# Kernel optimization log

Hardware: AMD Instinct MI355X
Metric: run time of the kernel (lower is better)

Reference implementation:

```python
import jax, jax.numpy as jnp
import numpy as np
from jax import lax

B, N, D, H, LAT, N_ENV = 8, 1024, 256, 8, 32, 64
HD = D // H


def _forward(x, conv_w, conv_b, phy_w, phy_b, to_out_w, to_out_b, env_keys,
             env_proj_w, env_proj_b, lambda_, q_w, q_b, k_w, k_b, v_w, v_b,
             out_proj_w, out_proj_b, gate_w, gate_b):
    b, n, d = x.shape
    h = H
    hd = d // h
    scale = hd ** -0.5
    hdim = int(np.sqrt(n))
    wdim = n // hdim

    # ---- physics branch: conv3x3 -> global avg pool -> linear -> 2h scalars ----
    K2d = x.reshape(b, hdim, wdim, d).transpose(0, 3, 1, 2)  # (b, d, H, W)
    conv = lax.conv_general_dilated(K2d, conv_w, (1, 1), ((1, 1), (1, 1)),
                                    dimension_numbers=('NCHW', 'OIHW', 'NCHW'))
    conv = conv + conv_b[None, :, None, None]
    pooled = conv.mean(axis=(2, 3))                 # (b, LAT)
    phy = pooled @ phy_w.T + phy_b                  # (b, 2h)
    atten = phy[:, :h][:, :, None, None]            # (b, h, 1, 1)
    scat = phy[:, h:][:, :, None, None]

    # ---- main physics-modulated attention (q=k=v=x, unprojected) ----
    q = x.reshape(b, n, h, hd).transpose(0, 2, 1, 3)  # (b, h, n, hd)
    k = q * (1.0 / (atten + 1e-6))
    dots = jnp.einsum('bhnd,bhmd->bhnm', q, k) * scale
    dots = dots * scat
    attn = jax.nn.softmax(dots, axis=-1)
    out = jnp.einsum('bhnm,bhmd->bhnd', attn, q)      # v == q here
    out = out.transpose(0, 2, 1, 3).reshape(b, n, d)
    out = out @ to_out_w.T + to_out_b

    # ---- env-memory branch (faithful to source: dim0 treated as tgt_len,
    #      dim1 as batch, so attention runs across the batch axis) ----
    n_env = env_keys.shape[0]
    q_e = (x @ q_w.T + q_b).reshape(b, n * h, hd).transpose(1, 0, 2)  # (n*h, b, hd)
    k_e = (x @ k_w.T + k_b).reshape(b, n * h, hd).transpose(1, 0, 2)
    v_e = (x @ v_w.T + v_b).reshape(b, n * h, hd).transpose(1, 0, 2)
    env_k = env_keys @ env_proj_w.T + env_proj_b                       # (n_env, d)
    env_k_bh = jnp.broadcast_to(env_k[:, None, :], (n_env, n, d))
    env_k_bh = env_k_bh.reshape(n_env, n * h, hd).transpose(1, 0, 2)   # (n*h, n_env, hd)

    attn_score = jnp.einsum('zbd,zcd->zbc', q_e, k_e)                  # (n*h, b, b)
    env_score = jnp.einsum('zbd,zed->zbe', q_e, env_k_bh)              # (n*h, b, n_env)
    combined = jnp.concatenate([attn_score, lambda_ * env_score], axis=-1)
    combined = jax.nn.softmax(combined / (hd ** 0.5), axis=-1)
    aw = combined[..., :b]
    ew = combined[..., b:]

    # env values: note (h, n) flattening order as in source permute/reshape
    env_v = jnp.broadcast_to(env_k.reshape(n_env, h, hd)[:, None, :, :],
                             (n_env, n, h, hd))
    env_v = env_v.transpose(2, 1, 0, 3).reshape(n * h, n_env, hd)

    out_e = jnp.einsum('zbc,zcd->zbd', aw, v_e) + jnp.einsum('zbe,zed->zbd', ew, env_v)
    out_e = out_e.transpose(1, 0, 2).reshape(b, n, d)
    out_e = out_e @ out_proj_w.T + out_proj_b

    # ---- gated fusion ----
    g = jax.nn.sigmoid(jnp.concatenate([out, out_e], axis=-1) @ gate_w.T + gate_b)
    return g * out + (1.0 - g) * out_e


def setup_inputs() -> dict:
    key = jax.random.key(0)
    ks = jax.random.split(key, 16)
    rn = lambda k, s: (jax.random.normal(k, s, dtype=jnp.float32) * 0.02)
    return {
        'x': jax.random.normal(ks[0], (B, N, D), dtype=jnp.float32),
        'conv_w': rn(ks[1], (LAT, D, 3, 3)),
        'conv_b': jnp.zeros((LAT,), jnp.float32),
        'phy_w': rn(ks[2], (2 * H, LAT)),
        'phy_b': jnp.ones((2 * H,), jnp.float32),  # keep attenuation ~1 for stability
        'to_out_w': rn(ks[3], (D, D)),
        'to_out_b': jnp.zeros((D,), jnp.float32),
        'env_keys': jax.random.normal(ks[4], (N_ENV, D), dtype=jnp.float32),
        'env_proj_w': rn(ks[5], (D, D)),
        'env_proj_b': jnp.zeros((D,), jnp.float32),
        'lambda_': jnp.asarray(0.5, jnp.float32),
        'q_w': rn(ks[6], (D, D)), 'q_b': jnp.zeros((D,), jnp.float32),
        'k_w': rn(ks[7], (D, D)), 'k_b': jnp.zeros((D,), jnp.float32),
        'v_w': rn(ks[8], (D, D)), 'v_b': jnp.zeros((D,), jnp.float32),
        'out_proj_w': rn(ks[9], (D, D)),
        'out_proj_b': jnp.zeros((D,), jnp.float32),
        'gate_w': rn(ks[10], (D, 2 * D)),
        'gate_b': jnp.zeros((D,), jnp.float32),
    }


def reference(x, conv_w, conv_b, phy_w, phy_b, to_out_w, to_out_b, env_keys,
              env_proj_w, env_proj_b, lambda_, q_w, q_b, k_w, k_b, v_w, v_b,
              out_proj_w, out_proj_b, gate_w, gate_b):
    return _forward(x, conv_w, conv_b, phy_w, phy_b, to_out_w, to_out_b,
                    env_keys, env_proj_w, env_proj_b, lambda_, q_w, q_b,
                    k_w, k_b, v_w, v_b, out_proj_w, out_proj_b, gate_w, gate_b)
```

## Files before the change

### kernel.cpp

```cpp
#include <hip/hip_runtime.h>
#include <hip/hip_bf16.h>
#include <cstdint>
#include <cstddef>

#define NB 8
#define NN 1024
#define ND 256
#define NH 8
#define HD 32

typedef __attribute__((ext_vector_type(8))) short bf16x8;
typedef __attribute__((ext_vector_type(4))) float f32x4;

static __device__ __forceinline__ float dot4(float4 a, float4 b) {
    return a.x * b.x + a.y * b.y + a.z * b.z + a.w * b.w;
}

static __device__ __forceinline__ uint32_t pack2bf(float x, float y) {
    __hip_bfloat16 bx = __float2bfloat16(x), by = __float2bfloat16(y);
    return (uint32_t)(*reinterpret_cast<uint16_t*>(&bx)) |
           ((uint32_t)(*reinterpret_cast<uint16_t*>(&by)) << 16);
}

static __device__ __forceinline__ ushort bf1(float x) {
    __hip_bfloat16 b = __float2bfloat16(x);
    return *reinterpret_cast<ushort*>(&b);
}

__global__ __launch_bounds__(256) void conv_sums_k(const float* __restrict__ x,
                                                   float* __restrict__ S) {
    const int b = blockIdx.y;
    const int q = blockIdx.x;
    const int c = threadIdx.x;
    const float* xb = x + (size_t)b * (NN * ND) + c;
    float T = 0.f, R0 = 0.f, R31 = 0.f, C0 = 0.f, C31 = 0.f;
    float c00 = 0.f, c0N = 0.f, cN0 = 0.f, cNN = 0.f;
    const int n0 = q * 64;
    for (int nn = 0; nn < 64; ++nn) {
        const int n = n0 + nn;
        const float v = xb[(size_t)n * ND];
        T += v;
        if (n < 32)   R0 += v;
        if (n >= 992) R31 += v;
        const int j = n & 31;
        if (j == 0)  C0 += v;
        if (j == 31) C31 += v;
        if (n == 0)    c00 = v;
        if (n == 31)   c0N = v;
        if (n == 992)  cN0 = v;
        if (n == 1023) cNN = v;
    }
    float* Sp = S + (size_t)b * 2304 + c * 9;
    atomicAdd(&Sp[0], T - R31 - C31 + cNN);
    atomicAdd(&Sp[1], T - R31);
    atomicAdd(&Sp[2], T - R31 - C0 + cN0);
    atomicAdd(&Sp[3], T - C31);
    atomicAdd(&Sp[4], T);
    atomicAdd(&Sp[5], T - C0);
    atomicAdd(&Sp[6], T - R0 - C31 + c0N);
    atomicAdd(&Sp[7], T - R0);
    atomicAdd(&Sp[8], T - R0 - C0 + c00);
}

__global__ __launch_bounds__(64) void pooled_k(const float* __restrict__ S,
                                               const float* __restrict__ conv_w,
                                               const float* __restrict__ conv_b,
                                               float* __restrict__ pooled) {
    const int bx = blockIdx.x;
    const int b = bx >> 5, o = bx & 31;
    const int t = threadIdx.x;
    const float4* w4 = (const float4*)(conv_w + (size_t)o * 2304);
    const float4* s4 = (const float4*)(S + (size_t)b * 2304);
    float acc = 0.f;
#pragma unroll
    for (int f = 0; f < 9; ++f) acc += dot4(w4[f * 64 + t], s4[f * 64 + t]);
    acc += __shfl_xor(acc, 1);  acc += __shfl_xor(acc, 2);
    acc += __shfl_xor(acc, 4);  acc += __shfl_xor(acc, 8);
    acc += __shfl_xor(acc, 16); acc += __shfl_xor(acc, 32);
    if (t == 0) pooled[b * 32 + o] = conv_b[o] + acc * (1.f / 1024.f);
}

__global__ __launch_bounds__(64) void phy_coef_k(const float* __restrict__ pooled,
                                                 const float* __restrict__ phy_w,
                                                 const float* __restrict__ phy_b,
                                                 float* __restrict__ coef) {
    __shared__ float ps[8][32];
    const int t = threadIdx.x;
#pragma unroll
    for (int r = 0; r < 4; ++r) {
        const int idx = r * 64 + t;
        ps[idx >> 5][idx & 31] = pooled[idx];
    }
    __syncthreads();
    const int b = t & 7, hh = t >> 3;
    float atten = phy_b[hh], scat = phy_b[8 + hh];
#pragma unroll
    for (int l = 0; l < 32; ++l) {
        atten += ps[b][l] * phy_w[hh * 32 + l];
        scat  += ps[b][l] * phy_w[(8 + hh) * 32 + l];
    }
    coef[b * 8 + hh] = 0.17677669529663687f * scat / (atten + 1e-6f);
}

__global__ __launch_bounds__(256) void phys_attn_mfma_k(const float* __restrict__ x,
                                                        const float* __restrict__ coef,
                                                        float* __restrict__ attn_out) {
    const int bh = blockIdx.y;
    const int b = bh >> 3, h = bh & 7;
    const int wv = threadIdx.x >> 6, lane = threadIdx.x & 63;
    const int g = lane >> 4, c16 = lane & 15;
    const float cf = coef[bh];
    const float* xb = x + (size_t)b * (NN * ND) + h * HD;

    __shared__ ushort Kl[2][32][40];
    __shared__ ushort VT[2][32][40];

    bf16x8 qf[2];
    const int q0 = blockIdx.x * 128 + wv * 32;
#pragma unroll
    for (int fq = 0; fq < 2; ++fq) {
        const float* qr = xb + (size_t)(q0 + fq * 16 + c16) * ND + g * 8;
        const float4 v0 = *(const float4*)&qr[0];
        const float4 v1 = *(const float4*)&qr[4];
        union { bf16x8 v; uint32_t u[4]; } qq;
        qq.u[0] = pack2bf(v0.x * cf, v0.y * cf);
        qq.u[1] = pack2bf(v0.z * cf, v0.w * cf);
        qq.u[2] = pack2bf(v1.x * cf, v1.y * cf);
        qq.u[3] = pack2bf(v1.z * cf, v1.w * cf);
        qf[fq] = qq.v;
    }

    const int skv = threadIdx.x >> 3, sdq = (threadIdx.x & 7) * 4;
    {
        const float4 v = *(const float4*)&xb[(size_t)skv * ND + sdq];
        const ushort e0 = bf1(v.x), e1 = bf1(v.y), e2 = bf1(v.z), e3 = bf1(v.w);
        uint2 kw; kw.x = (uint32_t)e0 | ((uint32_t)e1 << 16);
        kw.y = (uint32_t)e2 | ((uint32_t)e3 << 16);
        *(uint2*)&Kl[0][skv][sdq] = kw;
        VT[0][sdq + 0][skv] = e0; VT[0][sdq + 1][skv] = e1;
        VT[0][sdq + 2][skv] = e2; VT[0][sdq + 3][skv] = e3;
    }
    __syncthreads();

    f32x4 oacc[2][2];
#pragma unroll
    for (int i = 0; i < 2; ++i)
#pragma unroll
        for (int j = 0; j < 2; ++j) oacc[i][j] = (f32x4){0.f, 0.f, 0.f, 0.f};
    float m[2] = {-3.0e38f, -3.0e38f};
    float lsum[2] = {0.f, 0.f};

    const int srcA = c16 + (((2 * g) & 3) << 4);
    const int srcB = c16 + (((2 * g + 1) & 3) << 4);
    const int srcQ = (lane & 48) | (g * 4);

    for (int c = 0; c < 16 * 2; ++c) {
        const int cur = c & 1;
        float4 nv;
        const bool hasNext = (c + 1 < 32);
        if (hasNext)
            nv = *(const float4*)&xb[(size_t)((c + 1) * 32 + skv) * ND + sdq];

        const bf16x8 af0 = *(const bf16x8*)&Kl[cur][c16][g * 8];
        const bf16x8 af1 = *(const bf16x8*)&Kl[cur][16 + c16][g * 8];
        f32x4 sacc[2][2];
        const f32x4 z4 = (f32x4){0.f, 0.f, 0.f, 0.f};
        sacc[0][0] = __builtin_amdgcn_mfma_f32_16x16x32_bf16(af0, qf[0], z4, 0, 0, 0);
        sacc[0][1] = __builtin_amdgcn_mfma_f32_16x16x32_bf16(af0, qf[1], z4, 0, 0, 0);
        sacc[1][0] = __builtin_amdgcn_mfma_f32_16x16x32_bf16(af1, qf[0], z4, 0, 0, 0);
        sacc[1][1] = __builtin_amdgcn_mfma_f32_16x16x32_bf16(af1, qf[1], z4, 0, 0, 0);

        bf16x8 pa[2];
        float corrS[2];
#pragma unroll
        for (int fq = 0; fq < 2; ++fq) {
            float vmax = sacc[0][fq][0];
#pragma unroll
            for (int j = 1; j < 4; ++j) vmax = fmaxf(vmax, sacc[0][fq][j]);
#pragma unroll
            for (int j = 0; j < 4; ++j) vmax = fmaxf(vmax, sacc[1][fq][j]);
            vmax = fmaxf(vmax, __shfl_xor(vmax, 16));
            vmax = fmaxf(vmax, __shfl_xor(vmax, 32));
            const float mn = fmaxf(m[fq], vmax);
            corrS[fq] = __expf(m[fq] - mn);
            m[fq] = mn;
            float p[2][4];
            float rs = 0.f;
#pragma unroll
            for (int fkv = 0; fkv < 2; ++fkv)
#pragma unroll
                for (int j = 0; j < 4; ++j) {
                    p[fkv][j] = __expf(sacc[fkv][fq][j] - mn);
                    rs += p[fkv][j];
                }
            rs += __shfl_xor(rs, 16);
            rs += __shfl_xor(rs, 32);
            lsum[fq] = lsum[fq] * corrS[fq] + rs;

            uint32_t pk00 = pack2bf(p[0][0], p[0][1]);
            uint32_t pk01 = pack2bf(p[0][2], p[0][3]);
            uint32_t pk10 = pack2bf(p[1][0], p[1][1]);
            uint32_t pk11 = pack2bf(p[1][2], p[1][3]);
            const int t00 = __shfl((int)pk00, srcA), t10 = __shfl((int)pk10, srcA);
            const int t01 = __shfl((int)pk01, srcA), t11 = __shfl((int)pk11, srcA);
            const int t02 = __shfl((int)pk00, srcB), t12 = __shfl((int)pk10, srcB);
            const int t03 = __shfl((int)pk01, srcB), t13 = __shfl((int)pk11, srcB);
            union { bf16x8 v; uint32_t u[4]; } pu;
            const bool hi = (g >> 1) != 0;
            pu.u[0] = (uint32_t)(hi ? t10 : t00);
            pu.u[1] = (uint32_t)(hi ? t11 : t01);
            pu.u[2] = (uint32_t)(hi ? t12 : t02);
            pu.u[3] = (uint32_t)(hi ? t13 : t03);
            pa[fq] = pu.v;
        }

#pragma unroll
        for (int fq = 0; fq < 2; ++fq) {
#pragma unroll
            for (int j = 0; j < 4; ++j) {
                const float cj = __shfl(corrS[fq], srcQ + j);
                oacc[fq][0][j] *= cj;
                oacc[fq][1][j] *= cj;
            }
        }

        const bf16x8 bv0 = *(const bf16x8*)&VT[cur][c16][g * 8];
        const bf16x8 bv1 = *(const bf16x8*)&VT[cur][16 + c16][g * 8];
        oacc[0][0] = __builtin_amdgcn_mfma_f32_16x16x32_bf16(pa[0], bv0, oacc[0][0], 0, 0, 0);
        oacc[0][1] = __builtin_amdgcn_mfma_f32_16x16x32_bf16(pa[0], bv1, oacc[0][1], 0, 0, 0);
        oacc[1][0] = __builtin_amdgcn_mfma_f32_16x16x32_bf16(pa[1], bv0, oacc[1][0], 0, 0, 0);
        oacc[1][1] = __builtin_amdgcn_mfma_f32_16x16x32_bf16(pa[1], bv1, oacc[1][1], 0, 0, 0);

        if (hasNext) {
            const ushort e0 = bf1(nv.x), e1 = bf1(nv.y), e2 = bf1(nv.z), e3 = bf1(nv.w);
            uint2 kw; kw.x = (uint32_t)e0 | ((uint32_t)e1 << 16);
            kw.y = (uint32_t)e2 | ((uint32_t)e3 << 16);
            *(uint2*)&Kl[cur ^ 1][skv][sdq] = kw;
            VT[cur ^ 1][sdq + 0][skv] = e0; VT[cur ^ 1][sdq + 1][skv] = e1;
            VT[cur ^ 1][sdq + 2][skv] = e2; VT[cur ^ 1][sdq + 3][skv] = e3;
        }
        __syncthreads();
    }

#pragma unroll
    for (int fq = 0; fq < 2; ++fq) {
        const float inv = 1.f / lsum[fq];
#pragma unroll
        for (int j = 0; j < 4; ++j) {
            const float iv = __shfl(inv, srcQ + j);
            const int row = q0 + fq * 16 + g * 4 + j;
            float* orow = attn_out + (size_t)(b * NN + row) * ND + h * HD;
            orow[c16]      = oacc[fq][0][j] * iv;
            orow[16 + c16] = oacc[fq][1][j] * iv;
        }
    }
}

__global__ __launch_bounds__(256) void gemm_tn_k(const float* __restrict__ A,
                                                 const float* __restrict__ W,
                                                 const float* __restrict__ bias,
                                                 float* __restrict__ C,
                                                 int M, int N, int K) {
    __shared__ __align__(16) float As[32][64];
    __shared__ __align__(16) float Ws[32][64];
    const int tid = threadIdx.x;
    const int m0 = blockIdx.x * 64, n0 = blockIdx.y * 64;
    const int tx = tid & 15, ty = tid >> 4;
    const int lrow = tid >> 2, lc4 = (tid & 3) * 4;
    float acc[4][4] = {{0.f}};
    for (int k0 = 0; k0 < K; k0 += 32) {
        {
            const float* a = A + (size_t)(m0 + lrow) * K + k0 + lc4;
            const float4 v0 = *(const float4*)&a[0];
            const float4 v1 = *(const float4*)&a[16];
            As[lc4 + 0][lrow] = v0.x; As[lc4 + 1][lrow] = v0.y;
            As[lc4 + 2][lrow] = v0.z; As[lc4 + 3][lrow] = v0.w;
            As[lc4 + 16][lrow] = v1.x; As[lc4 + 17][lrow] = v1.y;
            As[lc4 + 18][lrow] = v1.z; As[lc4 + 19][lrow] = v1.w;
            const float* w = W + (size_t)(n0 + lrow) * K + k0 + lc4;
            const float4 u0 = *(const float4*)&w[0];
            const float4 u1 = *(const float4*)&w[16];
            Ws[lc4 + 0][lrow] = u0.x; Ws[lc4 + 1][lrow] = u0.y;
            Ws[lc4 + 2][lrow] = u0.z; Ws[lc4 + 3][lrow] = u0.w;
            Ws[lc4 + 16][lrow] = u1.x; Ws[lc4 + 17][lrow] = u1.y;
            Ws[lc4 + 18][lrow] = u1.z; Ws[lc4 + 19][lrow] = u1.w;
        }
        __syncthreads();
#pragma unroll
        for (int kk = 0; kk < 32; ++kk) {
            const float4 av = *(const float4*)&As[kk][ty * 4];
            const float4 wv = *(const float4*)&Ws[kk][tx * 4];
            const float a_[4] = {av.x, av.y, av.z, av.w};
            const float w_[4] = {wv.x, wv.y, wv.z, wv.w};
#pragma unroll
            for (int ri = 0; ri < 4; ++ri)
#pragma unroll
                for (int ci = 0; ci < 4; ++ci)
                    acc[ri][ci] = fmaf(a_[ri], w_[ci], acc[ri][ci]);
        }
        __syncthreads();
    }
#pragma unroll
    for (int ri = 0; ri < 4; ++ri)
#pragma unroll
        for (int ci = 0; ci < 4; ++ci) {
            const int row = m0 + ty * 4 + ri, col = n0 + tx * 4 + ci;
            C[(size_t)row * N + col] = acc[ri][ci] + bias[col];
        }
}

template <int GATE>
__global__ __launch_bounds__(256) void mfma_gemm_k(const float* __restrict__ A,
                                                   const float* __restrict__ A2,
                                                   const float* __restrict__ W,
                                                   const float* __restrict__ bias,
                                                   float* __restrict__ C,
                                                   int M, int K) {
    __shared__ ushort As[64][72];
    __shared__ ushort Ws[64][72];
    const int tid = threadIdx.x;
    const int m0 = blockIdx.x * 64, n0 = blockIdx.y * 64;
    const int w = tid >> 6, lane = tid & 63;
    const int wr = w >> 1, wc = w & 1;
    const int lr = lane & 15, lk = (lane >> 4) * 8;
    const int srow = tid >> 2, sc16 = (tid & 3) * 16;
    const int lda = GATE ? 256 : K;

    f32x4 acc[2][2];
#pragma unroll
    for (int i = 0; i < 2; ++i)
#pragma unroll
        for (int j = 0; j < 2; ++j) acc[i][j] = (f32x4){0.f, 0.f, 0.f, 0.f};

    const int nk = K / 64;
    for (int kt = 0; kt < nk; ++kt) {
        const float* srcA;
        int ka;
        if (GATE) {
            if (kt < 4) { srcA = A;  ka = kt * 64; }
            else        { srcA = A2; ka = (kt - 4) * 64; }
        } else { srcA = A; ka = kt * 64; }

        {
            const float* pa = srcA + (size_t)(m0 + srow) * lda + ka + sc16;
            const float* pw = W + (size_t)(n0 + srow) * K + kt * 64 + sc16;
#pragma unroll
            for (int q = 0; q < 4; ++q) {
                const float4 va = *(const float4*)&pa[q * 4];
                uint2 ua; ua.x = pack2bf(va.x, va.y); ua.y = pack2bf(va.z, va.w);
                *(uint2*)&As[srow][sc16 + q * 4] = ua;
                const float4 vw = *(const float4*)&pw[q * 4];
                uint2 uw; uw.x = pack2bf(vw.x, vw.y); uw.y = pack2bf(vw.z, vw.w);
                *(uint2*)&Ws[srow][sc16 + q * 4] = uw;
            }
        }
        __syncthreads();
#pragma unroll
        for (int kk = 0; kk < 2; ++kk) {
            bf16x8 af[2], bfr[2];
#pragma unroll
            for (int fm = 0; fm < 2; ++fm)
                af[fm] = *(const bf16x8*)&As[wr * 32 + fm * 16 + lr][kk * 32 + lk];
#pragma unroll
            for (int fn = 0; fn < 2; ++fn)
                bfr[fn] = *(const bf16x8*)&Ws[wc * 32 + fn * 16 + lr][kk * 32 + lk];
#pragma unroll
            for (int fm = 0; fm < 2; ++fm)
#pragma unroll
                for (int fn = 0; fn < 2; ++fn)
                    acc[fm][fn] = __builtin_amdgcn_mfma_f32_16x16x32_bf16(
                        af[fm], bfr[fn], acc[fm][fn], 0, 0, 0);
        }
        __syncthreads();
    }

#pragma unroll
    for (int fm = 0; fm < 2; ++fm)
#pragma unroll
        for (int fn = 0; fn < 2; ++fn) {
#pragma unroll
            for (int j = 0; j < 4; ++j) {
                const int row = m0 + wr * 32 + fm * 16 + (lane >> 4) * 4 + j;
                const int col = n0 + wc * 32 + fn * 16 + lr;
                const float v = acc[fm][fn][j] + bias[col];
                if (GATE) {
                    const float g = 1.f / (1.f + __expf(-v));
                    const float o  = A[(size_t)row * 256 + col];
                    const float oe = A2[(size_t)row * 256 + col];
                    C[(size_t)row * 256 + col] = g * o + (1.f - g) * oe;
                } else {
                    C[(size_t)row * 256 + col] = v;
                }
            }
        }
}

__global__ __launch_bounds__(256) void env_attn_k(const float* __restrict__ Qp,
                                                  const float* __restrict__ Kp,
                                                  const float* __restrict__ Vp,
                                                  const float* __restrict__ envk,
                                                  const float* __restrict__ lam_p,
                                                  float* __restrict__ oute_pre) {
    const int gtid = blockIdx.x * 256 + threadIdx.x;
    const int z = gtid & 8191, b = gtid >> 13;
    const int i = z >> 3, j = z & 7, j2 = z >> 10;
    const float lam = lam_p[0];
    const float rs32 = 0.17677669529663687f;

    float4 q[8];
    const float* qrow = Qp + ((size_t)b * NN + i) * ND + j * HD;
#pragma unroll
    for (int t = 0; t < 8; ++t) q[t] = *(const float4*)&qrow[t * 4];

    float s[72];
    float mx = -3.0e38f;
#pragma unroll
    for (int c = 0; c < 8; ++c) {
        const float* kr = Kp + ((size_t)c * NN + i) * ND + j * HD;
        float d = 0.f;
#pragma unroll
        for (int t = 0; t < 8; ++t) d += dot4(q[t], *(const float4*)&kr[t * 4]);
        s[c] = d * rs32;
        mx = fmaxf(mx, s[c]);
    }
#pragma unroll
    for (int e = 0; e < 64; ++e) {
        const float* er = envk + (size_t)e * ND + j * HD;
        float d = 0.f;
#pragma unroll
        for (int t = 0; t < 8; ++t) d += dot4(q[t], *(const float4*)&er[t * 4]);
        s[8 + e] = lam * d * rs32;
        mx = fmaxf(mx, s[8 + e]);
    }
    float sum = 0.f;
#pragma unroll
    for (int k = 0; k < 72; ++k) { s[k] = __expf(s[k] - mx); sum += s[k]; }
    const float inv = 1.f / sum;

    float4 o[8];
#pragma unroll
    for (int t = 0; t < 8; ++t) o[t] = make_float4(0.f, 0.f, 0.f, 0.f);
#pragma unroll
    for (int c = 0; c < 8; ++c) {
        const float* vr = Vp + ((size_t)c * NN + i) * ND + j * HD;
        const float w = s[c] * inv;
#pragma unroll
        for (int t = 0; t < 8; ++t) {
            const float4 v = *(const float4*)&vr[t * 4];
            o[t].x += w * v.x; o[t].y += w * v.y; o[t].z += w * v.z; o[t].w += w * v.w;
        }
    }
#pragma unroll
    for (int e = 0; e < 64; ++e) {
        const float* er = envk + (size_t)e * ND + j2 * HD;
        const float w = s[8 + e] * inv;
#pragma unroll
        for (int t = 0; t < 8; ++t) {
            const float4 v = *(const float4*)&er[t * 4];
            o[t].x += w * v.x; o[t].y += w * v.y; o[t].z += w * v.z; o[t].w += w * v.w;
        }
    }
    float* orow = oute_pre + ((size_t)b * NN + i) * ND + j * HD;
#pragma unroll
    for (int t = 0; t < 8; ++t) *(float4*)&orow[t * 4] = o[t];
}

extern "C" void kernel_launch(void* const* d_in, const int* in_sizes, int n_in,
                              void* d_out, int out_size, void* d_ws, size_t ws_size,
                              hipStream_t stream) {
    const float* x          = (const float*)d_in[0];
    const float* conv_w     = (const float*)d_in[1];
    const float* conv_b     = (const float*)d_in[2];
    const float* phy_w      = (const float*)d_in[3];
    const float* phy_b      = (const float*)d_in[4];
    const float* to_out_w   = (const float*)d_in[5];
    const float* to_out_b   = (const float*)d_in[6];
    const float* env_keys   = (const float*)d_in[7];
    const float* env_proj_w = (const float*)d_in[8];
    const float* env_proj_b = (const float*)d_in[9];
    const float* lambda_    = (const float*)d_in[10];
    const float* q_w        = (const float*)d_in[11];
    const float* q_b        = (const float*)d_in[12];
    const float* k_w        = (const float*)d_in[13];
    const float* k_b        = (const float*)d_in[14];
    const float* v_w        = (const float*)d_in[15];
    const float* v_b        = (const float*)d_in[16];
    const float* out_proj_w = (const float*)d_in[17];
    const float* out_proj_b = (const float*)d_in[18];
    const float* gate_w     = (const float*)d_in[19];
    const float* gate_b     = (const float*)d_in[20];
    (void)in_sizes; (void)n_in; (void)out_size; (void)ws_size;

    float* ws     = (float*)d_ws;
    float* Sb     = ws;
    float* coefw  = Sb + 18432;
    float* pooledw= coefw + 64;
    float* envk   = pooledw + 256;
    float* bufA   = envk + 16384;
    float* bufB   = bufA + 2097152;
    float* bufC   = bufB + 2097152;
    float* bufD   = bufC + 2097152;
    float* Vp     = (float*)d_out;

    hipMemsetAsync(Sb, 0, 18432 * sizeof(float), stream);
    conv_sums_k<<<dim3(16, 8), 256, 0, stream>>>(x, Sb);
    pooled_k<<<256, 64, 0, stream>>>(Sb, conv_w, conv_b, pooledw);
    phy_coef_k<<<1, 64, 0, stream>>>(pooledw, phy_w, phy_b, coefw);

    phys_attn_mfma_k<<<dim3(8, 64), 256, 0, stream>>>(x, coefw, bufA);
    mfma_gemm_k<0><<<dim3(128, 4), 256, 0, stream>>>(bufA, nullptr, to_out_w,
                                                     to_out_b, bufB, 8192, 256);

    mfma_gemm_k<0><<<dim3(128, 4), 256, 0, stream>>>(x, nullptr, q_w, q_b, bufC,
                                                     8192, 256);
    mfma_gemm_k<0><<<dim3(128, 4), 256, 0, stream>>>(x, nullptr, k_w, k_b, bufD,
                                                     8192, 256);
    mfma_gemm_k<0><<<dim3(128, 4), 256, 0, stream>>>(x, nullptr, v_w, v_b, Vp,
                                                     8192, 256);
    gemm_tn_k<<<dim3(1, 4), 256, 0, stream>>>(env_keys, env_proj_w, env_proj_b,
                                              envk, 64, 256, 256);

    env_attn_k<<<256, 256, 0, stream>>>(bufC, bufD, Vp, envk, lambda_, bufA);
    mfma_gemm_k<0><<<dim3(128, 4), 256, 0, stream>>>(bufA, nullptr, out_proj_w,
                                                     out_proj_b, bufC, 8192, 256);

    mfma_gemm_k<1><<<dim3(128, 4), 256, 0, stream>>>(bufB, bufC, gate_w, gate_b,
                                                     (float*)d_out, 8192, 512);
}
```

Baseline: 347.0 us.

## Split env attention head dim across four lanes with shuffle reductions

The env-memory attention kernel now assigns four threads per (row, head) pair, each owning 8 of the 32 head-dim elements. Partial dot products are combined with xor shuffles, and the grid grows from 256 to 1024 blocks. The aim is more parallelism, fewer live registers per thread and better coalesced loads than the old one-thread-per-head layout. The cost is 144 shuffles per thread and softmax work that is repeated in all four lanes.

```diff
diff --git a/kernel.cpp b/kernel.cpp
--- a/kernel.cpp
+++ b/kernel.cpp
@@ -24,7 +24,7 @@
 
 static __device__ __forceinline__ ushort bf1(float x) {
     __hip_bfloat16 b = __float2bfloat16(x);
-    return *reinterpret_cast<ushort*>(&b);
+    return *reinterpret_cast<uint16_t*>(&b);
 }
 
 __global__ __launch_bounds__(256) void conv_sums_k(const float* __restrict__ x,
@@ -402,67 +402,69 @@
                                                   const float* __restrict__ lam_p,
                                                   float* __restrict__ oute_pre) {
     const int gtid = blockIdx.x * 256 + threadIdx.x;
-    const int z = gtid & 8191, b = gtid >> 13;
+    const int dq = gtid & 3;
+    const int z = (gtid >> 2) & 8191;
+    const int b = gtid >> 15;
     const int i = z >> 3, j = z & 7, j2 = z >> 10;
     const float lam = lam_p[0];
     const float rs32 = 0.17677669529663687f;
-
-    float4 q[8];
-    const float* qrow = Qp + ((size_t)b * NN + i) * ND + j * HD;
-#pragma unroll
-    for (int t = 0; t < 8; ++t) q[t] = *(const float4*)&qrow[t * 4];
+    const int dof = j * HD + dq * 8;
+
+    const float* qrow = Qp + ((size_t)b * NN + i) * ND + dof;
+    const float4 q0 = *(const float4*)&qrow[0];
+    const float4 q1 = *(const float4*)&qrow[4];
 
     float s[72];
+#pragma unroll
+    for (int c = 0; c < 8; ++c) {
+        const float* kr = Kp + ((size_t)c * NN + i) * ND + dof;
+        s[c] = dot4(q0, *(const float4*)&kr[0]) + dot4(q1, *(const float4*)&kr[4]);
+    }
+#pragma unroll
+    for (int e = 0; e < 64; ++e) {
+        const float* er = envk + (size_t)e * ND + dof;
+        s[8 + e] = dot4(q0, *(const float4*)&er[0]) + dot4(q1, *(const float4*)&er[4]);
+    }
+#pragma unroll
+    for (int k = 0; k < 72; ++k) {
+        s[k] += __shfl_xor(s[k], 1);
+        s[k] += __shfl_xor(s[k], 2);
+    }
     float mx = -3.0e38f;
 #pragma unroll
-    for (int c = 0; c < 8; ++c) {
-        const float* kr = Kp + ((size_t)c * NN + i) * ND + j * HD;
-        float d = 0.f;
-#pragma unroll
-        for (int t = 0; t < 8; ++t) d += dot4(q[t], *(const float4*)&kr[t * 4]);
-        s[c] = d * rs32;
-        mx = fmaxf(mx, s[c]);
-    }
-#pragma unroll
-    for (int e = 0; e < 64; ++e) {
-        const float* er = envk + (size_t)e * ND + j * HD;
-        float d = 0.f;
-#pragma unroll
-        for (int t = 0; t < 8; ++t) d += dot4(q[t], *(const float4*)&er[t * 4]);
-        s[8 + e] = lam * d * rs32;
-        mx = fmaxf(mx, s[8 + e]);
-    }
+    for (int c = 0; c < 8; ++c) { s[c] *= rs32; mx = fmaxf(mx, s[c]); }
+    const float lr32 = lam * rs32;
+#pragma unroll
+    for (int e = 0; e < 64; ++e) { s[8 + e] *= lr32; mx = fmaxf(mx, s[8 + e]); }
     float sum = 0.f;
 #pragma unroll
     for (int k = 0; k < 72; ++k) { s[k] = __expf(s[k] - mx); sum += s[k]; }
     const float inv = 1.f / sum;
 
-    float4 o[8];
-#pragma unroll
-    for (int t = 0; t < 8; ++t) o[t] = make_float4(0.f, 0.f, 0.f, 0.f);
+    float4 o0 = make_float4(0.f, 0.f, 0.f, 0.f);
+    float4 o1 = make_float4(0.f, 0.f, 0.f, 0.f);
 #pragma unroll
     for (int c = 0; c < 8; ++c) {
-        const float* vr = Vp + ((size_t)c * NN + i) * ND + j * HD;
+        const float* vr = Vp + ((size_t)c * NN + i) * ND + dof;
         const float w = s[c] * inv;
-#pragma unroll
-        for (int t = 0; t < 8; ++t) {
-            const float4 v = *(const float4*)&vr[t * 4];
-            o[t].x += w * v.x; o[t].y += w * v.y; o[t].z += w * v.z; o[t].w += w * v.w;
-        }
-    }
+        const float4 v0 = *(const float4*)&vr[0];
+        const float4 v1 = *(const float4*)&vr[4];
+        o0.x += w * v0.x; o0.y += w * v0.y; o0.z += w * v0.z; o0.w += w * v0.w;
+        o1.x += w * v1.x; o1.y += w * v1.y; o1.z += w * v1.z; o1.w += w * v1.w;
+    }
+    const int dof2 = j2 * HD + dq * 8;
 #pragma unroll
     for (int e = 0; e < 64; ++e) {
-        const float* er = envk + (size_t)e * ND + j2 * HD;
+        const float* er = envk + (size_t)e * ND + dof2;
         const float w = s[8 + e] * inv;
-#pragma unroll
-        for (int t = 0; t < 8; ++t) {
-            const float4 v = *(const float4*)&er[t * 4];
-            o[t].x += w * v.x; o[t].y += w * v.y; o[t].z += w * v.z; o[t].w += w * v.w;
-        }
-    }
-    float* orow = oute_pre + ((size_t)b * NN + i) * ND + j * HD;
-#pragma unroll
-    for (int t = 0; t < 8; ++t) *(float4*)&orow[t * 4] = o[t];
+        const float4 v0 = *(const float4*)&er[0];
+        const float4 v1 = *(const float4*)&er[4];
+        o0.x += w * v0.x; o0.y += w * v0.y; o0.z += w * v0.z; o0.w += w * v0.w;
+        o1.x += w * v1.x; o1.y += w * v1.y; o1.z += w * v1.z; o1.w += w * v1.w;
+    }
+    float* orow = oute_pre + ((size_t)b * NN + i) * ND + dof;
+    *(float4*)&orow[0] = o0;
+    *(float4*)&orow[4] = o1;
 }
 
 extern "C" void kernel_launch(void* const* d_in, const int* in_sizes, int n_in,
@@ -520,7 +522,7 @@
     gemm_tn_k<<<dim3(1, 4), 256, 0, stream>>>(env_keys, env_proj_w, env_proj_b,
                                               envk, 64, 256, 256);
 
-    env_attn_k<<<256, 256, 0, stream>>>(bufC, bufD, Vp, envk, lambda_, bufA);
+    env_attn_k<<<1024, 256, 0, stream>>>(bufC, bufD, Vp, envk, lambda_, bufA);
     mfma_gemm_k<0><<<dim3(128, 4), 256, 0, stream>>>(bufA, nullptr, out_proj_w,
                                                      out_proj_b, bufC, 8192, 256);
 
```

Measured after the change: 298.0 us. -14.1%, faster.
